# Kernel tuning notes

Hardware: AMD Instinct MI355X
Metric: run time of the kernel (lower is better)

Reference implementation:

```python
import jax, jax.numpy as jnp
import numpy as np

N = 4096  # number of nodes (matches fill_max of edge indices)


def _dense(edges, n):
    # edges: [2, E] int; dense {0,1} adjacency. Duplicate edges collapse (set semantics).
    return jnp.zeros((n, n), dtype=jnp.float32).at[edges[0], edges[1]].set(1.0)


def setup_inputs() -> dict:
    key = jax.random.key(0)
    ks = jax.random.split(key, 4)
    E = 200000
    mk = lambda k: jax.random.randint(k, (2, E), 0, N, dtype=jnp.int32)
    return {
        "A_pos_t": mk(ks[0]),
        "A_pos_tp1": mk(ks[1]),
        "A_neg_t": mk(ks[2]),
        "A_neg_tp1": mk(ks[3]),
    }


def reference(A_pos_t, A_pos_tp1, A_neg_t, A_neg_tp1):
    p_t = _dense(A_pos_t, N)
    p1 = _dense(A_pos_tp1, N)
    n_t = _dense(A_neg_t, N)
    n1 = _dense(A_neg_tp1, N)

    # edge_index_diff: set symmetric difference == elementwise xor of {0,1} adjacency
    xor_p = p_t + p1 - 2.0 * p_t * p1
    xor_n = n_t + n1 - 2.0 * n_t * n1

    # Balance theory triangle closure on (tp1) graphs.
    # sign(a,b): +1 if pos edge (pos checked first -> priority), -1 elif neg edge.
    sp = p1                      # positive-sign edge indicator
    sn = n1 * (1.0 - p1)         # negative-sign edge indicator (pos has priority)
    off = 1.0 - jnp.eye(N, dtype=jnp.float32)
    spo = sp * off               # exclude b==a / b==c (triples are distinct)
    sno = sn * off

    # number of 2-paths a->b->c with predicted sign +1 / -1
    M_same = spo @ spo + sno @ sno
    M_diff = spo @ sno + sno @ spo

    # the Python loop only infers edges (a,c) with a < c (orientations (i,j,k),(i,k,j),(j,i,k))
    tri = jnp.triu(jnp.ones((N, N), dtype=jnp.float32), k=1)

    ind_p = M_same * tri * (1.0 - p1)  # skip pairs already positively connected
    ind_n = M_diff * tri * (1.0 - n1)  # skip pairs already negatively connected

    # Output: [2, N, N]; entry = xor indicator + indirect-edge multiplicity count
    return jnp.stack([xor_p + ind_p, xor_n + ind_n])
```

## Files before the change

kernel.cpp:

```cpp
#include <hip/hip_runtime.h>


#define NN 4096
#define NW 128
#define MASK_BYTES ((size_t)NN * NW * 4)
#define MASK_WORDS ((size_t)NN * NW)

typedef unsigned int u32;
typedef __attribute__((ext_vector_type(4))) int int4v;
typedef __attribute__((ext_vector_type(4))) float f32x4;

__device__ __forceinline__ void gload_lds16(const char* g, char* l) {
    __builtin_amdgcn_global_load_lds(
        (const __attribute__((address_space(1))) void*)g,
        (__attribute__((address_space(3))) void*)l, 16, 0, 0);
}


__global__ void zero_ws(int4v* __restrict__ p) {
    p[blockIdx.x * 256 + threadIdx.x] = int4v{0, 0, 0, 0};
}

__global__ void scatter_all(const int* __restrict__ e0, const int* __restrict__ e1,
                            const int* __restrict__ e2, const int* __restrict__ e3,
                            int E0, int E1, int E2, int E3,
                            u32* __restrict__ ws) {
    int i = blockIdx.x * blockDim.x + threadIdx.x;
    u32* Pt = ws + 0 * MASK_WORDS;
    u32* P1 = ws + 1 * MASK_WORDS;
    u32* Nt = ws + 2 * MASK_WORDS;
    u32* N1 = ws + 3 * MASK_WORDS;
    if (i < E0) { int r = e0[i], c = e0[i + E0];
        atomicOr(&Pt[r * NW + (c >> 5)], 1u << (c & 31)); }
    if (i < E1) { int r = e1[i], c = e1[i + E1];
        atomicOr(&P1[r * NW + (c >> 5)], 1u << (c & 31)); }
    if (i < E2) { int r = e2[i], c = e2[i + E2];
        atomicOr(&Nt[r * NW + (c >> 5)], 1u << (c & 31)); }
    if (i < E3) { int r = e3[i], c = e3[i + E3];
        atomicOr(&N1[r * NW + (c >> 5)], 1u << (c & 31)); }
}

__device__ __forceinline__ int4v expand_e(u32 sp, u32 sn) {
    int4v E;
    #pragma unroll
    for (int i = 0; i < 4; i++) {
        u32 p = (((sp >> (4 * i)) & 0xFu) * 0x00204081u) & 0x01010101u;
        u32 n = (((sn >> (4 * i)) & 0xFu) * 0x00204081u) & 0x01010101u;
        E[i] = (int)(p | (n << 5));
    }
    return E;
}

__global__ void build_both(const u32* __restrict__ masks,
                           char* __restrict__ E, char* __restrict__ ET) {
    const u32* P  = masks + 1 * MASK_WORDS;
    const u32* Nm = masks + 3 * MASK_WORDS;
    if (blockIdx.x < 2048) {
        int w = blockIdx.x * 256 + threadIdx.x;
        u32 p = P[w];
        u32 n = Nm[w] & ~p;
        int a = w >> 7, col = w & 127;
        if ((a >> 5) == col) {
            u32 db = 1u << (a & 31);
            p &= ~db; n &= ~db;
        }
        char* dst = E + (size_t)a * NN + col * 32;
        *reinterpret_cast<int4v*>(dst)      = expand_e(p & 0xFFFFu, n & 0xFFFFu);
        *reinterpret_cast<int4v*>(dst + 16) = expand_e(p >> 16, n >> 16);
    } else {
        int gw = (blockIdx.x - 2048) * 4 + (threadIdx.x >> 6);
        int lane = threadIdx.x & 63;
        int ab = gw >> 7;
        int wc = gw & 127;
        u32 pw = P[(ab * 64 + lane) * NW + wc];
        u32 nw = Nm[(ab * 64 + lane) * NW + wc];
        u32 myp = 0, myn = 0;
        #pragma unroll
        for (int j = 0; j < 32; j++) {
            unsigned long long bp = __ballot((pw >> j) & 1u);
            unsigned long long bn = __ballot((nw >> j) & 1u);
            if ((lane & 31) == j) {
                myp = (lane < 32) ? (u32)bp : (u32)(bp >> 32);
                myn = (lane < 32) ? (u32)bn : (u32)(bn >> 32);
            }
        }
        u32 p = myp;
        u32 n = myn & ~p;
        int c = wc * 32 + (lane & 31);
        int abase = ab * 64 + (lane >> 5) * 32;
        if (c >= abase && c < abase + 32) {
            u32 db = 1u << (c - abase);
            p &= ~db; n &= ~db;
        }
        char* dst = ET + (size_t)c * NN + abase;
        *reinterpret_cast<int4v*>(dst)      = expand_e(p & 0xFFFFu, n & 0xFFFFu);
        *reinterpret_cast<int4v*>(dst + 16) = expand_e(p >> 16, n >> 16);
    }
}

__global__ __launch_bounds__(256, 2) void gemm_ep(
    const char* __restrict__ E, const char* __restrict__ ET,
    const u32* __restrict__ Pt, const u32* __restrict__ P1,
    const u32* __restrict__ Nt, const u32* __restrict__ N1,
    float* __restrict__ out)
{
    const int tid = threadIdx.x;
    const size_t plane = (size_t)NN * NN;

    int s_ = ((int)blockIdx.x & 7) * 66 + ((int)blockIdx.x >> 3);
    int by = (int)((65.0f - sqrtf(4225.0f - 8.0f * (float)s_)) * 0.5f);
    if (by > 31) by = 31;
    while (by > 0 && 32 * by - (by * (by - 1)) / 2 > s_) --by;
    while (32 * (by + 1) - ((by + 1) * by) / 2 <= s_) ++by;
    int bx = by + s_ - (32 * by - (by * (by - 1)) / 2);
    const int a0 = by << 7, c0 = bx << 7;

    __shared__ char LB[5][16384];

    const int wave = tid >> 6, lane = tid & 63;
    const int wr = (wave >> 1) * 64, wcol = (wave & 1) * 64;
    const int lr = lane & 15, lg = lane >> 4;

    const int rh = tid >> 2, ch = tid & 3;
    const int swz = (ch ^ ((rh >> 1) & 3)) << 4;
    const char* gA = E  + (size_t)(a0 + rh) * NN + swz;
    const char* gB = ET + (size_t)(c0 + rh) * NN + swz;
    const int l16 = tid * 16;

    int4v acc[4][4];
    int4v zero = {0, 0, 0, 0};
    #pragma unroll
    for (int m = 0; m < 4; m++)
        #pragma unroll
        for (int n = 0; n < 4; n++) acc[m][n] = zero;

    #define STAGE(b, t)                                                \
        do {                                                           \
            const int koff = (t) * 64;                                 \
            gload_lds16(gA + koff,           &LB[b][l16]);             \
            gload_lds16(gA + 64 * NN + koff, &LB[b][4096 + l16]);      \
            gload_lds16(gB + koff,           &LB[b][8192 + l16]);      \
            gload_lds16(gB + 64 * NN + koff, &LB[b][12288 + l16]);     \
        } while (0)

    #define COMPUTE(b)                                                         \
        do {                                                                   \
            int4v bf[4];                                                       \
            _Pragma("unroll")                                                  \
            for (int n = 0; n < 4; n++) {                                      \
                int rowb = wcol + n * 16 + lr;                                 \
                bf[n] = *reinterpret_cast<const int4v*>(&LB[b][                \
                    8192 + rowb * 64 + ((lg ^ ((rowb >> 1) & 3)) << 4)]);      \
            }                                                                  \
            __builtin_amdgcn_s_setprio(1);                                     \
            _Pragma("unroll")                                                  \
            for (int m = 0; m < 4; m++) {                                      \
                int rowa = wr + m * 16 + lr;                                   \
                int4v af = *reinterpret_cast<const int4v*>(&LB[b][             \
                    rowa * 64 + ((lg ^ ((rowa >> 1) & 3)) << 4)]);             \
                _Pragma("unroll")                                              \
                for (int n = 0; n < 4; n++)                                    \
                    acc[m][n] = __builtin_amdgcn_mfma_i32_16x16x64_i8(         \
                        af, bf[n], acc[m][n], 0, 0, 0);                        \
            }                                                                  \
            __builtin_amdgcn_s_setprio(0);                                     \
        } while (0)

    if (by != bx) {
        #pragma unroll 4
        for (int pass = 0; pass < 16; ++pass) {
            int e = pass * 1024 + tid * 4;
            int r = e >> 7, cc = e & 127;
            int widx = (c0 + r) * NW + ((a0 + cc) >> 5);
            int sh = cc & 31;
            u32 xp = (P1[widx] ^ Pt[widx]) >> sh;
            u32 xn = (N1[widx] ^ Nt[widx]) >> sh;
            f32x4 o0, o1;
            #pragma unroll
            for (int i = 0; i < 4; i++) {
                o0[i] = (float)((xp >> i) & 1u);
                o1[i] = (float)((xn >> i) & 1u);
            }
            size_t ob = (size_t)(c0 + r) * NN + a0 + cc;
            *reinterpret_cast<f32x4*>(out + ob) = o0;
            *reinterpret_cast<f32x4*>(out + plane + ob) = o1;
        }
    }

    STAGE(0, 0);
    STAGE(1, 1);
    STAGE(2, 2);
    asm volatile("s_waitcnt vmcnt(8)" ::: "memory");
    __builtin_amdgcn_s_barrier();

    int cur = 0;
    for (int t = 0; t < 61; ++t) {
        int nb = cur + 3; if (nb >= 5) nb -= 5;
        STAGE(nb, t + 3);
        COMPUTE(cur);
        asm volatile("s_waitcnt vmcnt(8)" ::: "memory");
        __builtin_amdgcn_s_barrier();
        cur = (cur == 4) ? 0 : cur + 1;
    }
    COMPUTE(cur);
    asm volatile("s_waitcnt vmcnt(4)" ::: "memory");
    __builtin_amdgcn_s_barrier();
    cur = (cur == 4) ? 0 : cur + 1;
    COMPUTE(cur);
    asm volatile("s_waitcnt vmcnt(0)" ::: "memory");
    __builtin_amdgcn_s_barrier();
    cur = (cur == 4) ? 0 : cur + 1;
    COMPUTE(cur);
    #undef STAGE
    #undef COMPUTE

    #pragma unroll
    for (int m = 0; m < 4; m++) {
        #pragma unroll
        for (int n = 0; n < 4; n++) {
            #pragma unroll
            for (int q = 0; q < 4; q++) {
                int a = a0 + wr + m * 16 + lg * 4 + q;
                int c = c0 + wcol + n * 16 + lr;
                int widx = a * NW + (c >> 5);
                int bit = c & 31;
                u32 p1 = (P1[widx] >> bit) & 1u;
                u32 n1 = (N1[widx] >> bit) & 1u;
                u32 pt = (Pt[widx] >> bit) & 1u;
                u32 nt = (Nt[widx] >> bit) & 1u;
                int av = acc[m][n][q];
                int Ms = (av & 31) + (av >> 10);
                int Md = (av >> 5) & 31;
                int o0 = (int)(pt ^ p1) + ((a < c && !p1) ? Ms : 0);
                int o1 = (int)(nt ^ n1) + ((a < c && !n1) ? Md : 0);
                size_t oi = (size_t)a * NN + c;
                out[oi] = (float)o0;
                out[plane + oi] = (float)o1;
            }
        }
    }
}

extern "C" void kernel_launch(void* const* d_in, const int* in_sizes, int n_in,
                              void* d_out, int out_size, void* d_ws, size_t ws_size,
                              hipStream_t stream) {
    char* ws = (char*)d_ws;
    u32* masks = (u32*)ws;
    u32* Pt = masks + 0 * MASK_WORDS;
    u32* P1 = masks + 1 * MASK_WORDS;
    u32* Nt = masks + 2 * MASK_WORDS;
    u32* N1 = masks + 3 * MASK_WORDS;
    char* E  = ws + 4 * MASK_BYTES;
    char* ET = E + (size_t)NN * NN;

    zero_ws<<<2048, 256, 0, stream>>>((int4v*)masks);

    int E0 = in_sizes[0] / 2, E1 = in_sizes[1] / 2;
    int E2 = in_sizes[2] / 2, E3 = in_sizes[3] / 2;
    int Emax = max(max(E0, E1), max(E2, E3));
    scatter_all<<<(Emax + 255) / 256, 256, 0, stream>>>(
        (const int*)d_in[0], (const int*)d_in[1], (const int*)d_in[2],
        (const int*)d_in[3], E0, E1, E2, E3, masks);

    build_both<<<4096, 256, 0, stream>>>(masks, E, ET);

    gemm_ep<<<528, 256, 0, stream>>>(E, ET, Pt, P1, Nt, N1, (float*)d_out);
}
```

Measured before the change: 139.9 us.

## Use 128x256 tiles with 512 threads and double-buffered LDS pipeline

Switches the GEMM from 128x128 tiles (528 blocks of 256 threads, 5-stage LDS ring) to 128x256 tiles (272 blocks of 512 threads, two LDS buffers). The wider tile increases reuse of the A rows and cuts block count, and the lower-triangle xor-only fill moves after the epilogue with a new coverage test. The trade-off is shallower prefetch, since a full vmcnt(0) wait before every barrier exposes more load latency. Launch bounds of (512,6) look unrealistic for the register and LDS footprint.

```diff
diff --git a/kernel.cpp b/kernel.cpp
--- a/kernel.cpp
+++ b/kernel.cpp
@@ -98,7 +98,7 @@
     }
 }
 
-__global__ __launch_bounds__(256, 2) void gemm_ep(
+__global__ __launch_bounds__(512, 6) void gemm_ep(
     const char* __restrict__ E, const char* __restrict__ ET,
     const u32* __restrict__ Pt, const u32* __restrict__ P1,
     const u32* __restrict__ Nt, const u32* __restrict__ N1,
@@ -107,25 +107,26 @@
     const int tid = threadIdx.x;
     const size_t plane = (size_t)NN * NN;
 
-    int s_ = ((int)blockIdx.x & 7) * 66 + ((int)blockIdx.x >> 3);
-    int by = (int)((65.0f - sqrtf(4225.0f - 8.0f * (float)s_)) * 0.5f);
-    if (by > 31) by = 31;
-    while (by > 0 && 32 * by - (by * (by - 1)) / 2 > s_) --by;
-    while (32 * (by + 1) - ((by + 1) * by) / 2 <= s_) ++by;
-    int bx = by + s_ - (32 * by - (by * (by - 1)) / 2);
-    const int a0 = by << 7, c0 = bx << 7;
-
-    __shared__ char LB[5][16384];
+    const int id = ((int)blockIdx.x & 7) * 34 + ((int)blockIdx.x >> 3);
+    int j = (int)((sqrtf(4.0f * (float)id + 1.0f) - 1.0f) * 0.5f);
+    if (j > 15) j = 15;
+    while (j > 0 && j * (j + 1) > id) --j;
+    while ((j + 1) * (j + 2) <= id) ++j;
+    const int i = id - j * (j + 1);
+    const int a0 = i << 7, c0 = j << 8;
+
+    __shared__ char LB[2][24576];
 
     const int wave = tid >> 6, lane = tid & 63;
-    const int wr = (wave >> 1) * 64, wcol = (wave & 1) * 64;
+    const int wr = (wave >> 2) * 64;
+    const int wcol = (wave & 3) * 64;
     const int lr = lane & 15, lg = lane >> 4;
 
-    const int rh = tid >> 2, ch = tid & 3;
-    const int swz = (ch ^ ((rh >> 1) & 3)) << 4;
-    const char* gA = E  + (size_t)(a0 + rh) * NN + swz;
-    const char* gB = ET + (size_t)(c0 + rh) * NN + swz;
-    const int l16 = tid * 16;
+    const int soff = (((tid & 3) ^ ((tid >> 3) & 3)) << 4);
+    const char* gA  = E  + (size_t)(a0 + (tid >> 2)) * NN + soff;
+    const char* gB0 = ET + (size_t)(c0 + (tid >> 2)) * NN + soff;
+    const char* gB1 = gB0 + (size_t)128 * NN;
+    const int t16 = tid * 16;
 
     int4v acc[4][4];
     int4v zero = {0, 0, 0, 0};
@@ -134,13 +135,12 @@
         #pragma unroll
         for (int n = 0; n < 4; n++) acc[m][n] = zero;
 
-    #define STAGE(b, t)                                                \
-        do {                                                           \
-            const int koff = (t) * 64;                                 \
-            gload_lds16(gA + koff,           &LB[b][l16]);             \
-            gload_lds16(gA + 64 * NN + koff, &LB[b][4096 + l16]);      \
-            gload_lds16(gB + koff,           &LB[b][8192 + l16]);      \
-            gload_lds16(gB + 64 * NN + koff, &LB[b][12288 + l16]);     \
+    #define STAGE(b, p)                                           \
+        do {                                                      \
+            const int koff = (p) * 64;                            \
+            gload_lds16(gA  + koff, &LB[b][t16]);                 \
+            gload_lds16(gB0 + koff, &LB[b][8192 + t16]);          \
+            gload_lds16(gB1 + koff, &LB[b][16384 + t16]);         \
         } while (0)
 
     #define COMPUTE(b)                                                         \
@@ -166,50 +166,18 @@
             __builtin_amdgcn_s_setprio(0);                                     \
         } while (0)
 
-    if (by != bx) {
-        #pragma unroll 4
-        for (int pass = 0; pass < 16; ++pass) {
-            int e = pass * 1024 + tid * 4;
-            int r = e >> 7, cc = e & 127;
-            int widx = (c0 + r) * NW + ((a0 + cc) >> 5);
-            int sh = cc & 31;
-            u32 xp = (P1[widx] ^ Pt[widx]) >> sh;
-            u32 xn = (N1[widx] ^ Nt[widx]) >> sh;
-            f32x4 o0, o1;
-            #pragma unroll
-            for (int i = 0; i < 4; i++) {
-                o0[i] = (float)((xp >> i) & 1u);
-                o1[i] = (float)((xn >> i) & 1u);
-            }
-            size_t ob = (size_t)(c0 + r) * NN + a0 + cc;
-            *reinterpret_cast<f32x4*>(out + ob) = o0;
-            *reinterpret_cast<f32x4*>(out + plane + ob) = o1;
-        }
-    }
-
     STAGE(0, 0);
-    STAGE(1, 1);
-    STAGE(2, 2);
-    asm volatile("s_waitcnt vmcnt(8)" ::: "memory");
-    __builtin_amdgcn_s_barrier();
-
-    int cur = 0;
-    for (int t = 0; t < 61; ++t) {
-        int nb = cur + 3; if (nb >= 5) nb -= 5;
-        STAGE(nb, t + 3);
-        COMPUTE(cur);
-        asm volatile("s_waitcnt vmcnt(8)" ::: "memory");
-        __builtin_amdgcn_s_barrier();
-        cur = (cur == 4) ? 0 : cur + 1;
-    }
-    COMPUTE(cur);
-    asm volatile("s_waitcnt vmcnt(4)" ::: "memory");
-    __builtin_amdgcn_s_barrier();
-    cur = (cur == 4) ? 0 : cur + 1;
-    COMPUTE(cur);
     asm volatile("s_waitcnt vmcnt(0)" ::: "memory");
     __builtin_amdgcn_s_barrier();
-    cur = (cur == 4) ? 0 : cur + 1;
+
+    int cur = 0;
+    for (int p = 0; p < 63; ++p) {
+        STAGE(cur ^ 1, p + 1);
+        COMPUTE(cur);
+        asm volatile("s_waitcnt vmcnt(0)" ::: "memory");
+        __builtin_amdgcn_s_barrier();
+        cur ^= 1;
+    }
     COMPUTE(cur);
     #undef STAGE
     #undef COMPUTE
@@ -239,6 +207,29 @@
             }
         }
     }
+
+    {
+        #pragma unroll 4
+        for (int pass = 0; pass < 16; ++pass) {
+            int e = pass * 2048 + tid * 4;
+            int rr = e >> 7, cc = e & 127;
+            int R = c0 + rr, C = a0 + cc;
+            if ((R >> 7) <= 2 * (C >> 8) + 1) continue;
+            int widx = R * NW + (C >> 5);
+            int sh = C & 31;
+            u32 xp = (P1[widx] ^ Pt[widx]) >> sh;
+            u32 xn = (N1[widx] ^ Nt[widx]) >> sh;
+            f32x4 o0, o1;
+            #pragma unroll
+            for (int v = 0; v < 4; v++) {
+                o0[v] = (float)((xp >> v) & 1u);
+                o1[v] = (float)((xn >> v) & 1u);
+            }
+            size_t ob = (size_t)R * NN + C;
+            *reinterpret_cast<f32x4*>(out + ob) = o0;
+            *reinterpret_cast<f32x4*>(out + plane + ob) = o1;
+        }
+    }
 }
 
 extern "C" void kernel_launch(void* const* d_in, const int* in_sizes, int n_in,
@@ -264,5 +255,5 @@
 
     build_both<<<4096, 256, 0, stream>>>(masks, E, ET);
 
-    gemm_ep<<<528, 256, 0, stream>>>(E, ET, Pt, P1, Nt, N1, (float*)d_out);
-}
+    gemm_ep<<<272, 512, 0, stream>>>(E, ET, Pt, P1, Nt, N1, (float*)d_out);
+}
```

Measured after the change: 428.9 us. +206.5%, slower.
